# Kernel optimization log

Hardware: AMD Instinct MI355X
Metric: run time of the kernel (lower is better)

## Reference

```python
import jax, jax.numpy as jnp
import numpy as np

KS = 7  # neighborhood kernel size

def _wn(v, g):
    # weight-normalized 1x1-conv weight: v [out,in], g [out]
    n = jnp.sqrt(jnp.sum(v * v, axis=1, keepdims=True))
    return v * (g[:, None] / n)

def _ln(x, gamma, beta, eps=1e-6):
    mu = jnp.mean(x, axis=-1, keepdims=True)
    var = jnp.mean(jnp.square(x - mu), axis=-1, keepdims=True)
    return (x - mu) * jax.lax.rsqrt(var + eps) * gamma + beta

def _up_nearest(c, H, W):
    # integer-factor nearest upsample on channels-last [B,h,w,C]
    rh, rw = H // c.shape[1], W // c.shape[2]
    return jnp.repeat(jnp.repeat(c, rh, axis=1), rw, axis=2)

def _adaln(x, cond, gamma, beta, v, g):
    xn = _ln(x, gamma, beta)
    cu = _up_nearest(jax.nn.silu(cond), x.shape[1], x.shape[2])
    ab = cu @ _wn(v, g).T
    a, b = jnp.split(ab, 2, axis=-1)
    return xn * (1.0 + a) + b

def _gate(x, cond, v, g):
    cu = _up_nearest(jax.nn.silu(cond), x.shape[1], x.shape[2])
    return x * (cu @ _wn(v, g).T)

def _neigh_idx(n, k):
    # NATTEN-style clamped window starts: each query sees exactly k in-bounds neighbors
    starts = np.clip(np.arange(n) - k // 2, 0, n - k)
    return jnp.asarray(starts[:, None] + np.arange(k))  # [n,k]

def _natten2d(x, w_qkv, b_qkv, w_out, b_out, n_heads):
    B, H, W, C = x.shape
    hd = C // n_heads
    qkv = x @ w_qkv.T + b_qkv
    q, k, v = jnp.split(qkv, 3, axis=-1)
    q = q.reshape(B, H, W, n_heads, hd)
    k = k.reshape(B, H, W, n_heads, hd)
    v = v.reshape(B, H, W, n_heads, hd)
    ih = _neigh_idx(H, KS)
    iw = _neigh_idx(W, KS)
    def gather(t):
        t = t[:, ih]            # [B,H,KS,W,nh,hd]
        t = t[:, :, :, iw]      # [B,H,KS,W,KS,nh,hd]
        t = jnp.transpose(t, (0, 1, 3, 5, 2, 4, 6))  # [B,H,W,nh,KS,KS,hd]
        return t.reshape(B, H, W, n_heads, KS * KS, hd)
    kn, vn = gather(k), gather(v)
    scale = jnp.asarray(1.0 / np.sqrt(hd), x.dtype)
    logits = jnp.einsum('bhwnd,bhwnkd->bhwnk', q, kn) * scale
    attn = jax.nn.softmax(logits, axis=-1)
    out = jnp.einsum('bhwnk,bhwnkd->bhwnd', attn, vn).reshape(B, H, W, C)
    return out @ w_out.T + b_out

def _mlp(x, w1, b1, w2, b2):
    return jax.nn.gelu(x @ w1.T + b1) @ w2.T + b2

def setup_inputs():
    key = jax.random.key(0)
    B, H, W, D, CD, NH = 2, 48, 48, 384, 384, 6
    ks = jax.random.split(key, 10)
    s = 0.02
    return dict(
        x=jax.random.normal(ks[0], (B, H, W, D), jnp.float32),
        cond=jax.random.normal(ks[1], (B, 6, 6, CD), jnp.float32),
        ln1_g=jnp.ones((D,), jnp.float32), ln1_b=jnp.zeros((D,), jnp.float32),
        ada1_v=jax.random.normal(ks[2], (2 * D, CD), jnp.float32) * s,
        ada1_g=jnp.ones((2 * D,), jnp.float32),
        ln2_g=jnp.ones((D,), jnp.float32), ln2_b=jnp.zeros((D,), jnp.float32),
        ada2_v=jax.random.normal(ks[3], (2 * D, CD), jnp.float32) * s,
        ada2_g=jnp.ones((2 * D,), jnp.float32),
        gate1_v=jax.random.normal(ks[4], (D, CD), jnp.float32) * s,
        gate1_g=jnp.ones((D,), jnp.float32),
        gate2_v=jax.random.normal(ks[5], (D, CD), jnp.float32) * s,
        gate2_g=jnp.ones((D,), jnp.float32),
        w_qkv=jax.random.normal(ks[6], (3 * D, D), jnp.float32) * s,
        b_qkv=jnp.zeros((3 * D,), jnp.float32),
        w_out=jax.random.normal(ks[7], (D, D), jnp.float32) * s,
        b_out=jnp.zeros((D,), jnp.float32),
        w_mlp1=jax.random.normal(ks[8], (4 * D, D), jnp.float32) * s,
        b_mlp1=jnp.zeros((4 * D,), jnp.float32),
        w_mlp2=jax.random.normal(ks[9], (D, 4 * D), jnp.float32) * s,
        b_mlp2=jnp.zeros((D,), jnp.float32),
        n_heads=NH,
    )

def reference(x, cond, ln1_g, ln1_b, ada1_v, ada1_g, ln2_g, ln2_b, ada2_v, ada2_g,
              gate1_v, gate1_g, gate2_v, gate2_g, w_qkv, b_qkv, w_out, b_out,
              w_mlp1, b_mlp1, w_mlp2, b_mlp2, n_heads):
    h = _adaln(x, cond, ln1_g, ln1_b, ada1_v, ada1_g)
    h = _natten2d(h, w_qkv, b_qkv, w_out, b_out, n_heads)
    h = _gate(h, cond, gate1_v, gate1_g)
    x = x + h
    h = _adaln(x, cond, ln2_g, ln2_b, ada2_v, ada2_g)
    h = _mlp(h, w_mlp1, b_mlp1, w_mlp2, b_mlp2)
    h = _gate(h, cond, gate2_v, gate2_g)
    return x + h
```

## Files before the change

### kernel.cpp

```cpp
#include <hip/hip_runtime.h>
#include <hip/hip_bf16.h>
#include <math.h>

#define NPIX 4608
#define D 384
#define CD 384
#define C3 1152
#define DMLP 1536
#define NCELL 72

typedef unsigned short u16;
typedef __attribute__((ext_vector_type(8))) short bf16x8;
typedef __attribute__((ext_vector_type(4))) float f32x4;

#define OFF_MOD   0
#define OFF_BIG   663552
#define OFF_HHI   28975104
#define OFF_HLO   32514048
#define OFF_AHI   36052992
#define OFF_ALO   39591936
#define OFF_MHI   43130880
#define OFF_MLO   57286656
#define OFF_WHI   71442432
#define OFF_WLO   74981376
#define BIGOFF_MODV_HI  0
#define BIGOFF_MODV_LO  1769472
#define BIGOFF_SC_HI    3538944
#define BIGOFF_SC_LO    3637248
#define BIGOFF_INVN     3735552
#define WOFF_QKV  0
#define WOFF_OUT  442368
#define WOFF_M1   589824
#define WOFF_M2   1179648

#define GLOAD16(g, l) __builtin_amdgcn_global_load_lds( \
    (const __attribute__((address_space(1))) unsigned int*)(g), \
    (__attribute__((address_space(3))) unsigned int*)(l), 16, 0, 0)

__device__ __forceinline__ float wsum(float v) {
    #pragma unroll
    for (int o = 32; o > 0; o >>= 1) v += __shfl_xor(v, o);
    return v;
}
__device__ __forceinline__ void split_bf16(float x, u16& h, u16& l) {
    __hip_bfloat16 bh = __float2bfloat16(x);
    float fh = __bfloat162float(bh);
    __hip_bfloat16 bl = __float2bfloat16(x - fh);
    h = *(u16*)&bh; l = *(u16*)&bl;
}

__global__ __launch_bounds__(256) void wconv_kernel(
    const float* __restrict__ wq, const float* __restrict__ wo,
    const float* __restrict__ w1, const float* __restrict__ w2,
    const float* __restrict__ a1v, const float* __restrict__ a2v,
    const float* __restrict__ g1v, const float* __restrict__ g2v,
    u16* __restrict__ whi, u16* __restrict__ wlo,
    u16* __restrict__ mvhi, u16* __restrict__ mvlo)
{
    int i4 = blockIdx.x * 256 + threadIdx.x;
    const float* src; int l4; u16 *dh, *dl; int o;
    if (i4 < 442368) {
        if (i4 < 110592)        { src = wq; l4 = i4; }
        else if (i4 < 147456)   { src = wo; l4 = i4 - 110592; }
        else if (i4 < 294912)   { src = w1; l4 = i4 - 147456; }
        else                    { src = w2; l4 = i4 - 294912; }
        dh = whi; dl = wlo; o = i4 * 4;
    } else {
        int j4 = i4 - 442368;
        if (j4 < 73728)         { src = a1v; l4 = j4; }
        else if (j4 < 147456)   { src = a2v; l4 = j4 - 73728; }
        else if (j4 < 184320)   { src = g1v; l4 = j4 - 147456; }
        else                    { src = g2v; l4 = j4 - 184320; }
        dh = mvhi; dl = mvlo; o = j4 * 4;
    }
    float4 v = ((const float4*)src)[l4];
    split_bf16(v.x, dh[o+0], dl[o+0]);
    split_bf16(v.y, dh[o+1], dl[o+1]);
    split_bf16(v.z, dh[o+2], dl[o+2]);
    split_bf16(v.w, dh[o+3], dl[o+3]);
}

__global__ __launch_bounds__(256) void modprep_kernel(
    const float* __restrict__ cond,
    const float* __restrict__ a1v, const float* __restrict__ a1g,
    const float* __restrict__ a2v, const float* __restrict__ a2g,
    const float* __restrict__ g1v, const float* __restrict__ g1g,
    const float* __restrict__ g2v, const float* __restrict__ g2g,
    float* __restrict__ invn, u16* __restrict__ schi, u16* __restrict__ sclo)
{
    int wid  = (blockIdx.x * blockDim.x + threadIdx.x) >> 6;
    int lane = threadIdx.x & 63;
    if (wid < 2304) {
        const float* V; float g; int r;
        if (wid < 768)        { r = wid;        V = a1v; g = a1g[r]; }
        else if (wid < 1536)  { r = wid - 768;  V = a2v; g = a2g[r]; }
        else if (wid < 1920)  { r = wid - 1536; V = g1v; g = g1g[r]; }
        else                  { r = wid - 1920; V = g2v; g = g2g[r]; }
        const float* vrow = V + r * CD;
        float nrm = 0.f;
        #pragma unroll
        for (int j = 0; j < 6; j++) {
            float v = vrow[lane + 64 * j];
            nrm += v * v;
        }
        nrm = wsum(nrm);
        if (lane == 0) invn[wid] = g / sqrtf(nrm);
    } else {
        int cell = wid - 2304;
        #pragma unroll
        for (int j = 0; j < 6; j++) {
            int k = lane + 64 * j;
            float val = 0.f;
            if (cell < NCELL) {
                float c = cond[cell * CD + k];
                val = c / (1.f + __expf(-c));
            }
            split_bf16(val, schi[cell * CD + k], sclo[cell * CD + k]);
        }
    }
}

__global__ __launch_bounds__(256) void modgemm_mfma(
    const u16* __restrict__ Ah, const u16* __restrict__ Al,
    const u16* __restrict__ Bh, const u16* __restrict__ Bl,
    const float* __restrict__ invn, float* __restrict__ mod)
{
    __shared__ u16 lds[24576];
    const int tid  = threadIdx.x;
    const int lane = tid & 63;
    const int wid  = tid >> 6;
    const int n0 = blockIdx.x * 64;
    const int K = 384, nt = 12;
    const int wr = wid >> 1, wc = wid & 1;

    const u16* gsrc[6];
    int loff[6];
    #pragma unroll
    for (int s = 0; s < 6; s++) {
        int c = tid + (s << 8);
        const u16* base; int ks, row;
        if (c < 512)        { ks = c >> 7;           row = c & 127; base = Ah + (size_t)row * K; }
        else if (c < 1024)  { int cc = c - 512;  ks = cc >> 7; row = cc & 127; base = Al + (size_t)row * K; }
        else if (c < 1280)  { int cc = c - 1024; ks = cc >> 6; row = cc & 63;  base = Bh + (size_t)(n0 + row) * K; }
        else                { int cc = c - 1280; ks = cc >> 6; row = cc & 63;  base = Bl + (size_t)(n0 + row) * K; }
        gsrc[s] = base + ks * 8;
        loff[s] = c * 8;
    }

    f32x4 acc[4][2] = {};
    const int ks = lane >> 4;
    const int fr = lane & 15;

    #pragma unroll
    for (int s = 0; s < 6; s++) GLOAD16(gsrc[s], &lds[loff[s]]);
    __syncthreads();

    int cur = 0;
    for (int kt = 0; kt < nt; kt++) {
        if (kt + 1 < nt) {
            int k0 = (kt + 1) << 5;
            int dbo = (cur ^ 1) * 12288;
            #pragma unroll
            for (int s = 0; s < 6; s++) GLOAD16(gsrc[s] + k0, &lds[dbo + loff[s]]);
        }
        const int b0 = cur * 12288;
        bf16x8 ah[4], al[4], bh[2], bl[2];
        #pragma unroll
        for (int m = 0; m < 4; m++) {
            int ai = b0 + (ks * 128 + wr * 64 + m * 16 + fr) * 8;
            ah[m] = *(const bf16x8*)&lds[ai];
            al[m] = *(const bf16x8*)&lds[4096 + ai];
        }
        #pragma unroll
        for (int n = 0; n < 2; n++) {
            int bi = b0 + (ks * 64 + wc * 32 + n * 16 + fr) * 8;
            bh[n] = *(const bf16x8*)&lds[8192 + bi];
            bl[n] = *(const bf16x8*)&lds[10240 + bi];
        }
        #pragma unroll
        for (int m = 0; m < 4; m++)
            #pragma unroll
            for (int n = 0; n < 2; n++) {
                acc[m][n] = __builtin_amdgcn_mfma_f32_16x16x32_bf16(ah[m], bh[n], acc[m][n], 0, 0, 0);
                acc[m][n] = __builtin_amdgcn_mfma_f32_16x16x32_bf16(ah[m], bl[n], acc[m][n], 0, 0, 0);
                acc[m][n] = __builtin_amdgcn_mfma_f32_16x16x32_bf16(al[m], bh[n], acc[m][n], 0, 0, 0);
            }
        __syncthreads();
        cur ^= 1;
    }

    const int r4 = ks * 4;
    #pragma unroll
    for (int m = 0; m < 4; m++) {
        #pragma unroll
        for (int n = 0; n < 2; n++) {
            #pragma unroll
            for (int j = 0; j < 4; j++) {
                int row = wr * 64 + m * 16 + r4 + j;
                int col = n0 + wc * 32 + n * 16 + fr;
                if (row < NCELL)
                    mod[(size_t)row * 2304 + col] = acc[m][n][j] * invn[col];
            }
        }
    }
}

__global__ __launch_bounds__(256) void adaln_kernel(
    const float* __restrict__ x,
    const float* __restrict__ gamma, const float* __restrict__ beta,
    const float* __restrict__ mod_ab,
    u16* __restrict__ ohi, u16* __restrict__ olo)
{
    int p    = (blockIdx.x * blockDim.x + threadIdx.x) >> 6;
    int lane = threadIdx.x & 63;
    int b  = p / 2304;
    int hh = (p / 48) % 48;
    int ww = p % 48;
    int cell = b * 36 + (hh >> 3) * 6 + (ww >> 3);

    const float* xr = x + (size_t)p * D;
    float v[6]; float s = 0.f, ss = 0.f;
    #pragma unroll
    for (int j = 0; j < 6; j++) {
        v[j] = xr[lane + 64 * j];
        s  += v[j];
        ss += v[j] * v[j];
    }
    s = wsum(s); ss = wsum(ss);
    float mu  = s * (1.f / 384.f);
    float var = ss * (1.f / 384.f) - mu * mu;
    float rs  = 1.f / sqrtf(var + 1e-6f);

    const float* ab = mod_ab + (size_t)cell * 2304;
    #pragma unroll
    for (int j = 0; j < 6; j++) {
        int d = lane + 64 * j;
        float xn = (v[j] - mu) * rs * gamma[d] + beta[d];
        float o  = xn * (1.f + ab[d]) + ab[384 + d];
        split_bf16(o, ohi[(size_t)p * D + d], olo[(size_t)p * D + d]);
    }
}

template <int EPI, int NS>
__global__ __launch_bounds__(256) void gemm_mfma(
    const u16* __restrict__ Ah, const u16* __restrict__ Al,
    const u16* __restrict__ Bh, const u16* __restrict__ Bl,
    const float* __restrict__ bias,
    float* __restrict__ Cf, u16* __restrict__ Ch, u16* __restrict__ Cl,
    int N, int K)
{
    __shared__ u16 lds[24576];
    const int tid  = threadIdx.x;
    const int lane = tid & 63;
    const int wid  = tid >> 6;

    const int nwg = gridDim.x;
    const int q = nwg >> 3, r = nwg & 7;
    const int xcd = blockIdx.x & 7, loc = blockIdx.x >> 3;
    const int wgid = (xcd < r ? xcd * (q + 1) : r * (q + 1) + (xcd - r) * q) + loc;

    const int nx = N >> 6;
    const int per = nx * 36;
    const int bz  = wgid / per;
    const int id2 = wgid - bz * per;
    const int by  = id2 / nx;
    const int bx  = id2 - by * nx;

    const int m0 = by * 128;
    const int n0 = bx * 64;
    const int kPer = K / NS;
    const int kbeg = bz * kPer;
    const int nt = kPer >> 5;

    const int wr = wid >> 1, wc = wid & 1;

    const u16* gsrc[6];
    int loff[6];
    #pragma unroll
    for (int s = 0; s < 6; s++) {
        int c = tid + (s << 8);
        const u16* base; int ks, row;
        if (c < 512)        { ks = c >> 7;           row = c & 127; base = Ah + (size_t)(m0 + row) * K; }
        else if (c < 1024)  { int cc = c - 512;  ks = cc >> 7; row = cc & 127; base = Al + (size_t)(m0 + row) * K; }
        else if (c < 1280)  { int cc = c - 1024; ks = cc >> 6; row = cc & 63;  base = Bh + (size_t)(n0 + row) * K; }
        else                { int cc = c - 1280; ks = cc >> 6; row = cc & 63;  base = Bl + (size_t)(n0 + row) * K; }
        gsrc[s] = base + ks * 8;
        loff[s] = c * 8;
    }

    f32x4 acc[4][2] = {};
    const int ks = lane >> 4;
    const int fr = lane & 15;

    #pragma unroll
    for (int s = 0; s < 6; s++) GLOAD16(gsrc[s] + kbeg, &lds[loff[s]]);
    __syncthreads();

    int cur = 0;
    for (int kt = 0; kt < nt; kt++) {
        if (kt + 1 < nt) {
            int k0 = kbeg + ((kt + 1) << 5);
            int dbo = (cur ^ 1) * 12288;
            #pragma unroll
            for (int s = 0; s < 6; s++) GLOAD16(gsrc[s] + k0, &lds[dbo + loff[s]]);
        }
        const int b0 = cur * 12288;
        bf16x8 ah[4], al[4], bh[2], bl[2];
        #pragma unroll
        for (int m = 0; m < 4; m++) {
            int ai = b0 + (ks * 128 + wr * 64 + m * 16 + fr) * 8;
            ah[m] = *(const bf16x8*)&lds[ai];
            al[m] = *(const bf16x8*)&lds[4096 + ai];
        }
        #pragma unroll
        for (int n = 0; n < 2; n++) {
            int bi = b0 + (ks * 64 + wc * 32 + n * 16 + fr) * 8;
            bh[n] = *(const bf16x8*)&lds[8192 + bi];
            bl[n] = *(const bf16x8*)&lds[10240 + bi];
        }
        #pragma unroll
        for (int m = 0; m < 4; m++)
            #pragma unroll
            for (int n = 0; n < 2; n++) {
                acc[m][n] = __builtin_amdgcn_mfma_f32_16x16x32_bf16(ah[m], bh[n], acc[m][n], 0, 0, 0);
                acc[m][n] = __builtin_amdgcn_mfma_f32_16x16x32_bf16(ah[m], bl[n], acc[m][n], 0, 0, 0);
                acc[m][n] = __builtin_amdgcn_mfma_f32_16x16x32_bf16(al[m], bh[n], acc[m][n], 0, 0, 0);
            }
        __syncthreads();
        cur ^= 1;
    }

    const int r4 = ks * 4;
    #pragma unroll
    for (int m = 0; m < 4; m++) {
        #pragma unroll
        for (int n = 0; n < 2; n++) {
            #pragma unroll
            for (int j = 0; j < 4; j++) {
                int row = m0 + wr * 64 + m * 16 + r4 + j;
                int col = n0 + wc * 32 + n * 16 + fr;
                float v = acc[m][n][j];
                if (EPI == 0) {
                    Cf[(size_t)row * N + col] = v + bias[col];
                } else if (EPI == 1) {
                    float t = v + bias[col];
                    float c = 0.7978845608028654f * (t + 0.044715f * t * t * t);
                    float e = __expf(2.f * c);
                    float th = (e - 1.f) / (e + 1.f);
                    float g = 0.5f * t * (1.f + th);
                    size_t idx = (size_t)row * N + col;
                    split_bf16(g, Ch[idx], Cl[idx]);
                } else {
                    Cf[((size_t)bz * NPIX + row) * N + col] = v;
                }
            }
        }
    }
}

__global__ __launch_bounds__(256) void reduce_gate(
    const float* __restrict__ part, const float* __restrict__ bias,
    const float* __restrict__ gate, const float* __restrict__ resid,
    float* __restrict__ out)
{
    int i4 = blockIdx.x * 256 + threadIdx.x;
    int row = i4 / 96, c4 = i4 % 96;
    int b  = row / 2304;
    int hh = (row / 48) % 48;
    int ww = row % 48;
    int cell = b * 36 + (hh >> 3) * 6 + (ww >> 3);

    const float4* P = (const float4*)part;
    float4 p0 = P[i4], p1 = P[i4 + 442368], p2 = P[i4 + 2 * 442368], p3 = P[i4 + 3 * 442368];
    float4 bb = ((const float4*)bias)[c4];
    float4 gg = ((const float4*)(gate + (size_t)cell * 2304))[c4];
    float4 rr = ((const float4*)resid)[i4];
    float4 o;
    o.x = rr.x + (p0.x + p1.x + p2.x + p3.x + bb.x) * gg.x;
    o.y = rr.y + (p0.y + p1.y + p2.y + p3.y + bb.y) * gg.y;
    o.z = rr.z + (p0.z + p1.z + p2.z + p3.z + bb.z) * gg.z;
    o.w = rr.w + (p0.w + p1.w + p2.w + p3.w + bb.w) * gg.w;
    ((float4*)out)[i4] = o;
}

__global__ __launch_bounds__(256) void natten_kernel(
    const float* __restrict__ qkv, u16* __restrict__ ohi, u16* __restrict__ olo)
{
    int wid  = (blockIdx.x * blockDim.x + threadIdx.x) >> 6;
    int lane = threadIdx.x & 63;
    int head = wid % 6;
    int p    = wid / 6;
    int b  = p / 2304;
    int hh = (p / 48) % 48;
    int ww = p % 48;
    int sh = hh - 3; sh = sh < 0 ? 0 : (sh > 41 ? 41 : sh);
    int sw = ww - 3; sw = sw < 0 ? 0 : (sw > 41 ? 41 : sw);
    int pb = b * 2304;

    const int n_sub = lane >> 3;
    const int d_sub = lane & 7;
    const int dof = head * 64 + d_sub * 8;

    int npo[7];
    #pragma unroll
    for (int t = 0; t < 7; t++) {
        int n = t * 8 + n_sub;
        int nn = n > 48 ? 48 : n;
        int nr = nn / 7, nc = nn - nr * 7;
        npo[t] = pb + (sh + nr) * 48 + (sw + nc);
    }

    const float* qp = qkv + (size_t)p * C3 + dof;
    float4 q0 = *(const float4*)qp;
    float4 q1 = *(const float4*)(qp + 4);
    q0.x *= 0.125f; q0.y *= 0.125f; q0.z *= 0.125f; q0.w *= 0.125f;
    q1.x *= 0.125f; q1.y *= 0.125f; q1.z *= 0.125f; q1.w *= 0.125f;

    float4 kk0[7], kk1[7];
    #pragma unroll
    for (int t = 0; t < 7; t++) {
        const float* kp = qkv + (size_t)npo[t] * C3 + 384 + dof;
        kk0[t] = *(const float4*)kp;
        kk1[t] = *(const float4*)(kp + 4);
    }
    __builtin_amdgcn_sched_barrier(0);

    float L[7];
    #pragma unroll
    for (int t = 0; t < 7; t++) {
        float d = q0.x * kk0[t].x + q0.y * kk0[t].y + q0.z * kk0[t].z + q0.w * kk0[t].w
                + q1.x * kk1[t].x + q1.y * kk1[t].y + q1.z * kk1[t].z + q1.w * kk1[t].w;
        d += __shfl_xor(d, 1);
        d += __shfl_xor(d, 2);
        d += __shfl_xor(d, 4);
        L[t] = (t * 8 + n_sub < 49) ? d : -INFINITY;
    }

    float4 vv0[7], vv1[7];
    #pragma unroll
    for (int t = 0; t < 7; t++) {
        const float* vp = qkv + (size_t)npo[t] * C3 + 768 + dof;
        vv0[t] = *(const float4*)vp;
        vv1[t] = *(const float4*)(vp + 4);
    }
    __builtin_amdgcn_sched_barrier(0);

    float m = L[0];
    #pragma unroll
    for (int t = 1; t < 7; t++) m = fmaxf(m, L[t]);
    m = fmaxf(m, __shfl_xor(m, 8));
    m = fmaxf(m, __shfl_xor(m, 16));
    m = fmaxf(m, __shfl_xor(m, 32));

    float w[7]; float s = 0.f;
    #pragma unroll
    for (int t = 0; t < 7; t++) {
        w[t] = (L[t] == -INFINITY) ? 0.f : __expf(L[t] - m);
        s += w[t];
    }
    s += __shfl_xor(s, 8);
    s += __shfl_xor(s, 16);
    s += __shfl_xor(s, 32);
    float inv = 1.f / s;
    #pragma unroll
    for (int t = 0; t < 7; t++) w[t] *= inv;

    float a0x = 0.f, a0y = 0.f, a0z = 0.f, a0w = 0.f;
    float a1x = 0.f, a1y = 0.f, a1z = 0.f, a1w = 0.f;
    #pragma unroll
    for (int t = 0; t < 7; t++) {
        float wn = w[t];
        a0x = fmaf(wn, vv0[t].x, a0x); a0y = fmaf(wn, vv0[t].y, a0y);
        a0z = fmaf(wn, vv0[t].z, a0z); a0w = fmaf(wn, vv0[t].w, a0w);
        a1x = fmaf(wn, vv1[t].x, a1x); a1y = fmaf(wn, vv1[t].y, a1y);
        a1z = fmaf(wn, vv1[t].z, a1z); a1w = fmaf(wn, vv1[t].w, a1w);
    }
    #pragma unroll
    for (int o = 8; o <= 32; o <<= 1) {
        a0x += __shfl_xor(a0x, o); a0y += __shfl_xor(a0y, o);
        a0z += __shfl_xor(a0z, o); a0w += __shfl_xor(a0w, o);
        a1x += __shfl_xor(a1x, o); a1y += __shfl_xor(a1y, o);
        a1z += __shfl_xor(a1z, o); a1w += __shfl_xor(a1w, o);
    }

    if (lane < 8) {
        float av[8] = {a0x, a0y, a0z, a0w, a1x, a1y, a1z, a1w};
        u16 hi8[8], lo8[8];
        #pragma unroll
        for (int i = 0; i < 8; i++) split_bf16(av[i], hi8[i], lo8[i]);
        size_t oi = (size_t)p * D + head * 64 + lane * 8;
        *(uint4*)(ohi + oi) = *(uint4*)hi8;
        *(uint4*)(olo + oi) = *(uint4*)lo8;
    }
}

extern "C" void kernel_launch(void* const* d_in, const int* in_sizes, int n_in,
                              void* d_out, int out_size, void* d_ws, size_t ws_size,
                              hipStream_t stream)
{
    (void)in_sizes; (void)n_in; (void)out_size; (void)ws_size;
    const float* x      = (const float*)d_in[0];
    const float* cond   = (const float*)d_in[1];
    const float* ln1_g  = (const float*)d_in[2];
    const float* ln1_b  = (const float*)d_in[3];
    const float* ada1_v = (const float*)d_in[4];
    const float* ada1_g = (const float*)d_in[5];
    const float* ln2_g  = (const float*)d_in[6];
    const float* ln2_b  = (const float*)d_in[7];
    const float* ada2_v = (const float*)d_in[8];
    const float* ada2_g = (const float*)d_in[9];
    const float* gate1_v = (const float*)d_in[10];
    const float* gate1_g = (const float*)d_in[11];
    const float* gate2_v = (const float*)d_in[12];
    const float* gate2_g = (const float*)d_in[13];
    const float* w_qkv  = (const float*)d_in[14];
    const float* b_qkv  = (const float*)d_in[15];
    const float* w_out  = (const float*)d_in[16];
    const float* b_out  = (const float*)d_in[17];
    const float* w_mlp1 = (const float*)d_in[18];
    const float* b_mlp1 = (const float*)d_in[19];
    const float* w_mlp2 = (const float*)d_in[20];
    const float* b_mlp2 = (const float*)d_in[21];

    char* ws = (char*)d_ws;
    float* mod  = (float*)(ws + OFF_MOD);
    float* big  = (float*)(ws + OFF_BIG);
    u16* h_hi   = (u16*)(ws + OFF_HHI);
    u16* h_lo   = (u16*)(ws + OFF_HLO);
    u16* a_hi   = (u16*)(ws + OFF_AHI);
    u16* a_lo   = (u16*)(ws + OFF_ALO);
    u16* m_hi   = (u16*)(ws + OFF_MHI);
    u16* m_lo   = (u16*)(ws + OFF_MLO);
    u16* w_hi   = (u16*)(ws + OFF_WHI);
    u16* w_lo   = (u16*)(ws + OFF_WLO);
    char* bigc  = ws + OFF_BIG;
    u16* mv_hi  = (u16*)(bigc + BIGOFF_MODV_HI);
    u16* mv_lo  = (u16*)(bigc + BIGOFF_MODV_LO);
    u16* sc_hi  = (u16*)(bigc + BIGOFF_SC_HI);
    u16* sc_lo  = (u16*)(bigc + BIGOFF_SC_LO);
    float* invn = (float*)(bigc + BIGOFF_INVN);
    float* x2   = (float*)d_out;

    wconv_kernel<<<2592, 256, 0, stream>>>(
        w_qkv, w_out, w_mlp1, w_mlp2, ada1_v, ada2_v, gate1_v, gate2_v,
        w_hi, w_lo, mv_hi, mv_lo);

    modprep_kernel<<<608, 256, 0, stream>>>(
        cond, ada1_v, ada1_g, ada2_v, ada2_g, gate1_v, gate1_g, gate2_v, gate2_g,
        invn, sc_hi, sc_lo);

    modgemm_mfma<<<36, 256, 0, stream>>>(sc_hi, sc_lo, mv_hi, mv_lo, invn, mod);

    adaln_kernel<<<NPIX / 4, 256, 0, stream>>>(x, ln1_g, ln1_b, mod, h_hi, h_lo);

    gemm_mfma<0, 1><<<648, 256, 0, stream>>>(
        h_hi, h_lo, w_hi + WOFF_QKV, w_lo + WOFF_QKV, b_qkv,
        big, nullptr, nullptr, C3, D);

    natten_kernel<<<(NPIX * 6) / 4, 256, 0, stream>>>(big, a_hi, a_lo);

    gemm_mfma<2, 4><<<864, 256, 0, stream>>>(
        a_hi, a_lo, w_hi + WOFF_OUT, w_lo + WOFF_OUT, nullptr,
        big, nullptr, nullptr, D, D);

    reduce_gate<<<1728, 256, 0, stream>>>(big, b_out, mod + 1536, x, x2);

    adaln_kernel<<<NPIX / 4, 256, 0, stream>>>(x2, ln2_g, ln2_b, mod + 768, h_hi, h_lo);

    gemm_mfma<1, 1><<<864, 256, 0, stream>>>(
        h_hi, h_lo, w_hi + WOFF_M1, w_lo + WOFF_M1, b_mlp1,
        nullptr, m_hi, m_lo, DMLP, D);

    gemm_mfma<2, 4><<<864, 256, 0, stream>>>(
        m_hi, m_lo, w_hi + WOFF_M2, w_lo + WOFF_M2, nullptr,
        big, nullptr, nullptr, D, DMLP);

    reduce_gate<<<1728, 256, 0, stream>>>(big, b_mlp2, mod + 1920, x2, x2);
}
```

Measured before the change: 331.4 us.

## Drop split-K, fuse bias/gate/residual into GEMM epilogue, shrink tiles to 64x64

The GEMM tile shrinks from 128x64 to 64x64 and split-K is removed, so the out-projection and MLP2 GEMMs compute full K per block. Bias, the per-cell gate and the residual add now happen in the GEMM epilogue, which eliminates the reduce_gate kernels and the fp32 partial-sum round trip. The natten kernel also gets an XCD-aware block swizzle. The trade-off is fewer blocks (432) and long K loops for the D-output GEMMs, plus less data reuse per tile.

```diff
diff --git a/kernel.cpp b/kernel.cpp
--- a/kernel.cpp
+++ b/kernel.cpp
@@ -241,15 +241,16 @@
     }
 }
 
-template <int EPI, int NS>
+template <int EPI>
 __global__ __launch_bounds__(256) void gemm_mfma(
     const u16* __restrict__ Ah, const u16* __restrict__ Al,
     const u16* __restrict__ Bh, const u16* __restrict__ Bl,
     const float* __restrict__ bias,
     float* __restrict__ Cf, u16* __restrict__ Ch, u16* __restrict__ Cl,
+    const float* __restrict__ gate, const float* __restrict__ resid,
     int N, int K)
 {
-    __shared__ u16 lds[24576];
+    __shared__ u16 lds[16384];
     const int tid  = threadIdx.x;
     const int lane = tid & 63;
     const int wid  = tid >> 6;
@@ -260,66 +261,62 @@
     const int wgid = (xcd < r ? xcd * (q + 1) : r * (q + 1) + (xcd - r) * q) + loc;
 
     const int nx = N >> 6;
-    const int per = nx * 36;
-    const int bz  = wgid / per;
-    const int id2 = wgid - bz * per;
-    const int by  = id2 / nx;
-    const int bx  = id2 - by * nx;
-
-    const int m0 = by * 128;
+    const int by = wgid / nx;
+    const int bx = wgid - by * nx;
+    const int m0 = by * 64;
     const int n0 = bx * 64;
-    const int kPer = K / NS;
-    const int kbeg = bz * kPer;
-    const int nt = kPer >> 5;
+    const int nt = K >> 5;
 
     const int wr = wid >> 1, wc = wid & 1;
 
-    const u16* gsrc[6];
-    int loff[6];
-    #pragma unroll
-    for (int s = 0; s < 6; s++) {
+    const u16* gsrc[4];
+    int loff[4];
+    #pragma unroll
+    for (int s = 0; s < 4; s++) {
         int c = tid + (s << 8);
-        const u16* base; int ks, row;
-        if (c < 512)        { ks = c >> 7;           row = c & 127; base = Ah + (size_t)(m0 + row) * K; }
-        else if (c < 1024)  { int cc = c - 512;  ks = cc >> 7; row = cc & 127; base = Al + (size_t)(m0 + row) * K; }
-        else if (c < 1280)  { int cc = c - 1024; ks = cc >> 6; row = cc & 63;  base = Bh + (size_t)(n0 + row) * K; }
-        else                { int cc = c - 1280; ks = cc >> 6; row = cc & 63;  base = Bl + (size_t)(n0 + row) * K; }
+        int ks = (c & 255) >> 6;
+        int row = c & 63;
+        const u16* base;
+        if (c < 256)       base = Ah + (size_t)(m0 + row) * K;
+        else if (c < 512)  base = Al + (size_t)(m0 + row) * K;
+        else if (c < 768)  base = Bh + (size_t)(n0 + row) * K;
+        else               base = Bl + (size_t)(n0 + row) * K;
         gsrc[s] = base + ks * 8;
         loff[s] = c * 8;
     }
 
-    f32x4 acc[4][2] = {};
+    f32x4 acc[2][2] = {};
     const int ks = lane >> 4;
     const int fr = lane & 15;
 
     #pragma unroll
-    for (int s = 0; s < 6; s++) GLOAD16(gsrc[s] + kbeg, &lds[loff[s]]);
+    for (int s = 0; s < 4; s++) GLOAD16(gsrc[s], &lds[loff[s]]);
     __syncthreads();
 
     int cur = 0;
     for (int kt = 0; kt < nt; kt++) {
         if (kt + 1 < nt) {
-            int k0 = kbeg + ((kt + 1) << 5);
-            int dbo = (cur ^ 1) * 12288;
+            int k0 = (kt + 1) << 5;
+            int dbo = (cur ^ 1) * 8192;
             #pragma unroll
-            for (int s = 0; s < 6; s++) GLOAD16(gsrc[s] + k0, &lds[dbo + loff[s]]);
-        }
-        const int b0 = cur * 12288;
-        bf16x8 ah[4], al[4], bh[2], bl[2];
-        #pragma unroll
-        for (int m = 0; m < 4; m++) {
-            int ai = b0 + (ks * 128 + wr * 64 + m * 16 + fr) * 8;
+            for (int s = 0; s < 4; s++) GLOAD16(gsrc[s] + k0, &lds[dbo + loff[s]]);
+        }
+        const int b0 = cur * 8192;
+        bf16x8 ah[2], al[2], bh[2], bl[2];
+        #pragma unroll
+        for (int m = 0; m < 2; m++) {
+            int ai = b0 + (ks * 64 + wr * 32 + m * 16 + fr) * 8;
             ah[m] = *(const bf16x8*)&lds[ai];
-            al[m] = *(const bf16x8*)&lds[4096 + ai];
+            al[m] = *(const bf16x8*)&lds[2048 + ai];
         }
         #pragma unroll
         for (int n = 0; n < 2; n++) {
             int bi = b0 + (ks * 64 + wc * 32 + n * 16 + fr) * 8;
-            bh[n] = *(const bf16x8*)&lds[8192 + bi];
-            bl[n] = *(const bf16x8*)&lds[10240 + bi];
-        }
-        #pragma unroll
-        for (int m = 0; m < 4; m++)
+            bh[n] = *(const bf16x8*)&lds[4096 + bi];
+            bl[n] = *(const bf16x8*)&lds[6144 + bi];
+        }
+        #pragma unroll
+        for (int m = 0; m < 2; m++)
             #pragma unroll
             for (int n = 0; n < 2; n++) {
                 acc[m][n] = __builtin_amdgcn_mfma_f32_16x16x32_bf16(ah[m], bh[n], acc[m][n], 0, 0, 0);
@@ -332,12 +329,12 @@
 
     const int r4 = ks * 4;
     #pragma unroll
-    for (int m = 0; m < 4; m++) {
+    for (int m = 0; m < 2; m++) {
         #pragma unroll
         for (int n = 0; n < 2; n++) {
             #pragma unroll
             for (int j = 0; j < 4; j++) {
-                int row = m0 + wr * 64 + m * 16 + r4 + j;
+                int row = m0 + wr * 32 + m * 16 + r4 + j;
                 int col = n0 + wc * 32 + n * 16 + fr;
                 float v = acc[m][n][j];
                 if (EPI == 0) {
@@ -351,42 +348,27 @@
                     size_t idx = (size_t)row * N + col;
                     split_bf16(g, Ch[idx], Cl[idx]);
                 } else {
-                    Cf[((size_t)bz * NPIX + row) * N + col] = v;
+                    int b  = row / 2304;
+                    int hh = (row / 48) % 48;
+                    int ww = row % 48;
+                    int cell = b * 36 + (hh >> 3) * 6 + (ww >> 3);
+                    size_t idx = (size_t)row * N + col;
+                    Cf[idx] = resid[idx] + (v + bias[col]) * gate[(size_t)cell * 2304 + col];
                 }
             }
         }
     }
 }
 
-__global__ __launch_bounds__(256) void reduce_gate(
-    const float* __restrict__ part, const float* __restrict__ bias,
-    const float* __restrict__ gate, const float* __restrict__ resid,
-    float* __restrict__ out)
-{
-    int i4 = blockIdx.x * 256 + threadIdx.x;
-    int row = i4 / 96, c4 = i4 % 96;
-    int b  = row / 2304;
-    int hh = (row / 48) % 48;
-    int ww = row % 48;
-    int cell = b * 36 + (hh >> 3) * 6 + (ww >> 3);
-
-    const float4* P = (const float4*)part;
-    float4 p0 = P[i4], p1 = P[i4 + 442368], p2 = P[i4 + 2 * 442368], p3 = P[i4 + 3 * 442368];
-    float4 bb = ((const float4*)bias)[c4];
-    float4 gg = ((const float4*)(gate + (size_t)cell * 2304))[c4];
-    float4 rr = ((const float4*)resid)[i4];
-    float4 o;
-    o.x = rr.x + (p0.x + p1.x + p2.x + p3.x + bb.x) * gg.x;
-    o.y = rr.y + (p0.y + p1.y + p2.y + p3.y + bb.y) * gg.y;
-    o.z = rr.z + (p0.z + p1.z + p2.z + p3.z + bb.z) * gg.z;
-    o.w = rr.w + (p0.w + p1.w + p2.w + p3.w + bb.w) * gg.w;
-    ((float4*)out)[i4] = o;
-}
-
 __global__ __launch_bounds__(256) void natten_kernel(
     const float* __restrict__ qkv, u16* __restrict__ ohi, u16* __restrict__ olo)
 {
-    int wid  = (blockIdx.x * blockDim.x + threadIdx.x) >> 6;
+    const int nwg = gridDim.x;
+    const int q8 = nwg >> 3, r8 = nwg & 7;
+    const int xcd = blockIdx.x & 7, loc = blockIdx.x >> 3;
+    const int bswz = (xcd < r8 ? xcd * (q8 + 1) : r8 * (q8 + 1) + (xcd - r8) * q8) + loc;
+
+    int wid  = bswz * 4 + (threadIdx.x >> 6);
     int lane = threadIdx.x & 63;
     int head = wid % 6;
     int p    = wid / 6;
@@ -553,27 +535,23 @@
 
     adaln_kernel<<<NPIX / 4, 256, 0, stream>>>(x, ln1_g, ln1_b, mod, h_hi, h_lo);
 
-    gemm_mfma<0, 1><<<648, 256, 0, stream>>>(
+    gemm_mfma<0><<<1296, 256, 0, stream>>>(
         h_hi, h_lo, w_hi + WOFF_QKV, w_lo + WOFF_QKV, b_qkv,
-        big, nullptr, nullptr, C3, D);
+        big, nullptr, nullptr, nullptr, nullptr, C3, D);
 
     natten_kernel<<<(NPIX * 6) / 4, 256, 0, stream>>>(big, a_hi, a_lo);
 
-    gemm_mfma<2, 4><<<864, 256, 0, stream>>>(
-        a_hi, a_lo, w_hi + WOFF_OUT, w_lo + WOFF_OUT, nullptr,
-        big, nullptr, nullptr, D, D);
-
-    reduce_gate<<<1728, 256, 0, stream>>>(big, b_out, mod + 1536, x, x2);
+    gemm_mfma<3><<<432, 256, 0, stream>>>(
+        a_hi, a_lo, w_hi + WOFF_OUT, w_lo + WOFF_OUT, b_out,
+        x2, nullptr, nullptr, mod + 1536, x, D, D);
 
     adaln_kernel<<<NPIX / 4, 256, 0, stream>>>(x2, ln2_g, ln2_b, mod + 768, h_hi, h_lo);
 
-    gemm_mfma<1, 1><<<864, 256, 0, stream>>>(
+    gemm_mfma<1><<<1728, 256, 0, stream>>>(
         h_hi, h_lo, w_hi + WOFF_M1, w_lo + WOFF_M1, b_mlp1,
-        nullptr, m_hi, m_lo, DMLP, D);
-
-    gemm_mfma<2, 4><<<864, 256, 0, stream>>>(
-        m_hi, m_lo, w_hi + WOFF_M2, w_lo + WOFF_M2, nullptr,
-        big, nullptr, nullptr, D, DMLP);
-
-    reduce_gate<<<1728, 256, 0, stream>>>(big, b_mlp2, mod + 1920, x2, x2);
-}
+        nullptr, m_hi, m_lo, nullptr, nullptr, DMLP, D);
+
+    gemm_mfma<3><<<432, 256, 0, stream>>>(
+        m_hi, m_lo, w_hi + WOFF_M2, w_lo + WOFF_M2, b_mlp2,
+        x2, nullptr, nullptr, mod + 1920, x2, D, DMLP);
+}
```

New measurement: 325.4 us. Within noise of the previous version (-1.8%).
